# Optimization experiments

Hardware: AMD Instinct MI355X
Metric: run time of the kernel (lower is better)

## Reference

```python
import jax, jax.numpy as jnp
import numpy as np
from jax import lax

# Fixed image shape (H, W) for all images, standard detection resize
H_IMG, W_IMG = 800.0, 1333.0
SCORE_THRESH = 0.05
NMS_THRESH = 0.5
DET_PER_IMG = 100
K_PRE = 2048  # NMS candidate budget per image (after score threshold)
BBOX_XFORM_CLIP = float(np.log(1000.0 / 16.0))
WX, WY, WW, WH = 10.0, 10.0, 5.0, 5.0  # bbox_reg_weights


def setup_inputs() -> dict:
    B, P, C = 8, 2000, 81
    key = jax.random.key(0)
    k1, k2, k3, k4 = jax.random.split(key, 4)
    class_logits = 2.0 * jax.random.normal(k1, (B * P, C), jnp.float32)
    box_regression = 0.5 * jax.random.normal(k2, (B * P, C * 4), jnp.float32)
    # valid proposal boxes inside the image: (x1,y1) + (w,h)
    xy = jax.random.uniform(k3, (B, P, 2), jnp.float32) * jnp.array([W_IMG - 128.0, H_IMG - 128.0], jnp.float32)
    wh = 1.0 + 127.0 * jax.random.uniform(k4, (B, P, 2), jnp.float32)
    proposals = jnp.concatenate([xy, xy + wh], axis=-1)
    return {"class_logits": class_logits, "box_regression": box_regression, "proposals": proposals}


def _decode(rel, boxes):
    # BoxCoder.decode: rel [N, C, 4], boxes [N, 4] -> [N, C, 4]
    w = boxes[:, 2] - boxes[:, 0]
    h = boxes[:, 3] - boxes[:, 1]
    cx = boxes[:, 0] + 0.5 * w
    cy = boxes[:, 1] + 0.5 * h
    dx = rel[..., 0] / WX
    dy = rel[..., 1] / WY
    dw = jnp.minimum(rel[..., 2] / WW, BBOX_XFORM_CLIP)
    dh = jnp.minimum(rel[..., 3] / WH, BBOX_XFORM_CLIP)
    pcx = dx * w[:, None] + cx[:, None]
    pcy = dy * h[:, None] + cy[:, None]
    pw = jnp.exp(dw) * w[:, None]
    ph = jnp.exp(dh) * h[:, None]
    return jnp.stack([pcx - 0.5 * pw, pcy - 0.5 * ph, pcx + 0.5 * pw, pcy + 0.5 * ph], axis=-1)


def _pairwise_iou(b):
    # b: [K, 4] -> [K, K]
    area = jnp.maximum(b[:, 2] - b[:, 0], 0.0) * jnp.maximum(b[:, 3] - b[:, 1], 0.0)
    lt = jnp.maximum(b[:, None, :2], b[None, :, :2])
    rb = jnp.minimum(b[:, None, 2:], b[None, :, 2:])
    wh = jnp.maximum(rb - lt, 0.0)
    inter = wh[..., 0] * wh[..., 1]
    union = area[:, None] + area[None, :] - inter
    return inter / jnp.maximum(union, 1e-9)


def _greedy_nms(boxes, valid):
    # boxes: [K, 4] sorted by score desc; valid: [K] bool. Exact greedy NMS.
    K = boxes.shape[0]
    iou = _pairwise_iou(boxes)
    idx = jnp.arange(K)

    def body(i, keep):
        sup = keep[i] & (iou[i] > NMS_THRESH) & (idx > i)
        return keep & ~sup

    return lax.fori_loop(0, K, body, valid)


def reference(class_logits, box_regression, proposals):
    B, P, _ = proposals.shape
    C = class_logits.shape[-1]
    # decode all class-specific boxes, softmax scores
    rel = box_regression.reshape(-1, C, 4)
    pred = _decode(rel, proposals.reshape(-1, 4)).reshape(B, P, C, 4)
    scores = jax.nn.softmax(class_logits, axis=-1).reshape(B, P, C)
    # drop background class 0
    M = P * (C - 1)
    boxes = pred[:, :, 1:, :].reshape(B, M, 4)
    scores = scores[:, :, 1:].reshape(B, M)
    labels = jnp.broadcast_to(jnp.arange(1, C)[None, None, :], (B, P, C - 1)).reshape(B, M)
    # clip to image
    x1 = jnp.clip(boxes[..., 0], 0.0, W_IMG)
    y1 = jnp.clip(boxes[..., 1], 0.0, H_IMG)
    x2 = jnp.clip(boxes[..., 2], 0.0, W_IMG)
    y2 = jnp.clip(boxes[..., 3], 0.0, H_IMG)
    boxes = jnp.stack([x1, y1, x2, y2], axis=-1)
    # score threshold + remove_small_boxes(min_size=0.01), as a validity mask
    valid = (scores > SCORE_THRESH) & ((x2 - x1) >= 0.01) & ((y2 - y1) >= 0.01)
    masked = jnp.where(valid, scores, -1.0)
    # top-K candidates per image (sorted desc -> NMS visiting order)
    top_s, top_i = lax.top_k(masked, K_PRE)
    top_b = jnp.take_along_axis(boxes, top_i[..., None], axis=1)
    top_l = jnp.take_along_axis(labels, top_i, axis=1)
    top_v = top_s > 0.0
    # batched_nms: per-class coordinate offsets so classes never overlap
    off = top_l.astype(jnp.float32) * (jnp.maximum(W_IMG, H_IMG) + 1.0)
    keep = jax.vmap(_greedy_nms)(top_b + off[..., None], top_v)
    final = jnp.where(keep, top_s, -1.0)
    det_s, det_i = lax.top_k(final, DET_PER_IMG)
    det_b = jnp.take_along_axis(top_b, det_i[..., None], axis=1)
    det_l = jnp.take_along_axis(top_l, det_i, axis=1)
    det_valid = det_s > 0.0  # padding slots have score -1
    return det_b, det_s, det_l, det_valid
```

## Files before the change

### kernel.cpp

```cpp
#include <hip/hip_runtime.h>
#include <cstdint>
#include <cstddef>

typedef unsigned long long u64;

constexpr int Bn   = 8;
constexpr int Pn   = 2000;
constexpr int Cn   = 81;
constexpr int CM1  = 80;
constexpr int KPRE = 2048;
constexpr int NDET = 100;
constexpr int SECP = 8;
constexpr int NSEC2 = Pn / SECP;
constexpr int SSLOT = 160;
constexpr int CAP  = 4096;
constexpr int NBINS = 5632;
constexpr int BINOFF = (122 << 10);
constexpr float W_IMG = 1333.0f;
constexpr float H_IMG = 800.0f;
constexpr float XFORM_CLIP = 4.135166556742356f;
constexpr float NMS_OFF = 1334.0f;

constexpr size_t OFF_HIST = 0;
constexpr size_t ZERO_BYTES = (size_t)Bn * NBINS * 4;
constexpr size_t OFF_SL   = ZERO_BYTES;
constexpr size_t OFF_SC   = OFF_SL + (size_t)Bn * NSEC2 * SSLOT * 8;
constexpr size_t OFF_CANDA = OFF_SC + (size_t)Bn * NSEC2 * 4;

__device__ __forceinline__ void decode_clip(const float4 rv, float w, float h,
                                            float cx, float cy, float out[4]) {
  float dx = rv.x / 10.0f;
  float dy = rv.y / 10.0f;
  float dw = fminf(rv.z / 5.0f, XFORM_CLIP);
  float dh = fminf(rv.w / 5.0f, XFORM_CLIP);
  float pcx = dx * w + cx;
  float pcy = dy * h + cy;
  float pw = expf(dw) * w;
  float ph = expf(dh) * h;
  out[0] = fminf(fmaxf(pcx - 0.5f * pw, 0.0f), W_IMG);
  out[1] = fminf(fmaxf(pcy - 0.5f * ph, 0.0f), H_IMG);
  out[2] = fminf(fmaxf(pcx + 0.5f * pw, 0.0f), W_IMG);
  out[3] = fminf(fmaxf(pcy + 0.5f * ph, 0.0f), H_IMG);
}

__device__ __forceinline__ int score_bin(unsigned bits) {
  int bin = (int)(bits >> 13) - BINOFF;
  return min(max(bin, 0), NBINS - 1);
}

__device__ __forceinline__ void key_decode(u64 key, int b,
                                           const float* __restrict__ reg,
                                           const float* __restrict__ props,
                                           float bx[4], int& label, float& sc) {
  sc = __uint_as_float((unsigned)(key >> 32));
  bx[0] = bx[1] = bx[2] = bx[3] = 0.0f;
  label = 0;
  if (key != 0ull) {
    int m = (int)(0xFFFFFFFFu - (unsigned)key);
    int p = m / CM1;
    int c = m - p * CM1 + 1;
    int nidx = b * Pn + p;
    const float4 pb = *reinterpret_cast<const float4*>(props + (size_t)nidx * 4);
    float w = pb.z - pb.x, h = pb.w - pb.y;
    float cx = pb.x + 0.5f * w, cy = pb.y + 0.5f * h;
    float4 rv = *reinterpret_cast<const float4*>(reg + (size_t)nidx * (Cn * 4) + c * 4);
    decode_clip(rv, w, h, cx, cy, bx);
    label = c;
  }
}

__global__ __launch_bounds__(256) void
k1_score(const float* __restrict__ logits, const float* __restrict__ reg,
         const float* __restrict__ props, u64* __restrict__ slices,
         int* __restrict__ scnt, int* __restrict__ hist) {
  int blk = blockIdx.x, t = threadIdx.x, lane = t & 63, wv = t >> 6;
  int b = blk / NSEC2, sec = blk % NSEC2;
  __shared__ u64 cbuf[SSLOT];
  __shared__ int cnt_sh;
  if (t == 0) cnt_sh = 0;
  __syncthreads();
  int* hrow = hist + (size_t)b * NBINS;

  #pragma unroll
  for (int pp = wv; pp < SECP; pp += 4) {
    int p = sec * SECP + pp;
    int wid = b * Pn + p;
    const float* lg = logits + (size_t)wid * Cn;
    float x0 = lg[lane];
    float x1 = (lane < Cn - 64) ? lg[64 + lane] : -3.4e38f;
    float mx = fmaxf(x0, x1);
    for (int m = 32; m; m >>= 1) mx = fmaxf(mx, __shfl_xor(mx, m, 64));
    float e0 = expf(x0 - mx);
    float e1 = (lane < Cn - 64) ? expf(x1 - mx) : 0.0f;
    float ssum = e0 + e1;
    for (int m = 32; m; m >>= 1) ssum += __shfl_xor(ssum, m, 64);

    const float4 pb = *reinterpret_cast<const float4*>(props + (size_t)wid * 4);
    float w = pb.z - pb.x, h = pb.w - pb.y;
    float cx = pb.x + 0.5f * w, cy = pb.y + 0.5f * h;
    const float* rrow = reg + (size_t)wid * (Cn * 4);

    u64 key0 = 0ull, key1 = 0ull;
    if (lane >= 1) {
      float sc = e0 / ssum;
      if (sc > 0.05f) {
        float4 rv = *reinterpret_cast<const float4*>(rrow + lane * 4);
        float bx[4];
        decode_clip(rv, w, h, cx, cy, bx);
        if ((bx[2] - bx[0] >= 0.01f) && (bx[3] - bx[1] >= 0.01f)) {
          unsigned m = (unsigned)(p * CM1 + (lane - 1));
          key0 = ((u64)__float_as_uint(sc) << 32) | (0xFFFFFFFFu - m);
        }
      }
    }
    if (lane < Cn - 64) {
      int c = 64 + lane;
      float sc = e1 / ssum;
      if (sc > 0.05f) {
        float4 rv = *reinterpret_cast<const float4*>(rrow + c * 4);
        float bx[4];
        decode_clip(rv, w, h, cx, cy, bx);
        if ((bx[2] - bx[0] >= 0.01f) && (bx[3] - bx[1] >= 0.01f)) {
          unsigned m = (unsigned)(p * CM1 + (c - 1));
          key1 = ((u64)__float_as_uint(sc) << 32) | (0xFFFFFFFFu - m);
        }
      }
    }
    u64 bal0 = __ballot(key0 != 0ull);
    u64 bal1 = __ballot(key1 != 0ull);
    int tot = __popcll(bal0) + __popcll(bal1);
    if (tot) {
      int base = 0;
      if (lane == 0) base = atomicAdd(&cnt_sh, tot);
      base = __shfl(base, 0, 64);
      int r0 = __popcll(bal0 & ((1ull << lane) - 1ull));
      int r1 = __popcll(bal0) + __popcll(bal1 & ((1ull << lane) - 1ull));
      if (key0) {
        cbuf[base + r0] = key0;
        atomicAdd(&hrow[score_bin((unsigned)(key0 >> 32))], 1);
      }
      if (key1) {
        cbuf[base + r1] = key1;
        atomicAdd(&hrow[score_bin((unsigned)(key1 >> 32))], 1);
      }
    }
  }
  __syncthreads();
  int n = cnt_sh;
  for (int i = t; i < n; i += 256) slices[(size_t)blk * SSLOT + i] = cbuf[i];
  if (t == 0) scnt[blk] = n;
}

template <int CHV>
__device__ __forceinline__ void mp_round(u64* buf, int base, int nA, int nB,
                                         int outLen, int tid) {
  const u64* A = buf + base;
  const u64* B = buf + base + nA;
  int d = tid * CHV;
  u64 rg[CHV];
  int cnt = 0;
  if (d < outLen) {
    int lo = max(0, d - nB), hi = min(d, nA);
    while (lo < hi) {
      int mid = (lo + hi) >> 1;
      if (A[mid] >= B[d - 1 - mid]) lo = mid + 1; else hi = mid;
    }
    int i = lo, j = d - lo;
    for (int e = 0; e < CHV && d + e < outLen; e++) {
      u64 v;
      if (j >= nB || (i < nA && A[i] >= B[j])) v = A[i++];
      else v = B[j++];
      rg[cnt++] = v;
    }
  }
  __syncthreads();
  for (int e = 0; e < cnt; e++) buf[base + d + e] = rg[e];
  __syncthreads();
}

__global__ __launch_bounds__(1024) void
k2_fused(const int* __restrict__ hist, const u64* __restrict__ slices,
         const int* __restrict__ scnt, u64* __restrict__ candA,
         const float* __restrict__ reg, const float* __restrict__ props,
         float* __restrict__ out) {
  int b = blockIdx.x, t = threadIdx.x, lane = t & 63, w = t >> 6;
  __shared__ u64 bufA[CAP];
  __shared__ u64 maskb[256][4];
  __shared__ u64 keepw[KPRE / 64];
  __shared__ int accI[NDET];
  __shared__ int kcnt_sh;
  __shared__ int partial[256];
  __shared__ int sufAfter[256];
  __shared__ int lcnt[NSEC2];
  __shared__ int tmax_sh, cnt_sh;
  float4* obox = (float4*)bufA;

  for (int i = t; i < CAP; i += 1024) bufA[i] = 0ull;

  const int CH = NBINS / 256;
  const int* hrow = hist + (size_t)b * NBINS;
  if (t == 0) { tmax_sh = 0; cnt_sh = 0; }
  if (t < 256) {
    int lo = t * CH, hi = lo + CH;
    int s = 0;
    for (int i = lo; i < hi; i++) s += hrow[i];
    partial[t] = s;
  }
  if (t < NSEC2) lcnt[t] = scnt[b * NSEC2 + t];
  __syncthreads();
  if (t < 256) sufAfter[t] = partial[t];
  __syncthreads();
  for (int s = 1; s < 256; s <<= 1) {
    int y = 0;
    if (t < 256 && t + s < 256) y = sufAfter[t + s];
    __syncthreads();
    if (t < 256) sufAfter[t] += y;
    __syncthreads();
  }
  if (t < 256) {
    int lo = t * CH, hi = lo + CH;
    int cum = (t + 1 < 256) ? sufAfter[t + 1] : 0;
    int cand = -1;
    for (int i = hi - 1; i >= lo; i--) {
      cum += hrow[i];
      if (cum >= KPRE) { cand = i; break; }
    }
    if (cand >= 0) atomicMax(&tmax_sh, cand);
  }
  __syncthreads();
  int T = tmax_sh;

  for (int sec = w; sec < NSEC2; sec += 16) {
    int n = lcnt[sec];
    const u64* sl = slices + (size_t)(b * NSEC2 + sec) * SSLOT;
    for (int i0 = 0; i0 < n; i0 += 64) {
      int i = i0 + lane;
      u64 key = (i < n) ? sl[i] : 0ull;
      bool pass = key && (score_bin((unsigned)(key >> 32)) >= T);
      u64 bal = __ballot(pass);
      int tot = __popcll(bal);
      if (tot) {
        int base = 0;
        if (lane == 0) base = atomicAdd(&cnt_sh, tot);
        base = __shfl(base, 0, 64);
        int rank = __popcll(bal & ((1ull << lane) - 1ull));
        int pos = base + rank;
        if (pass && pos < CAP) bufA[pos] = key;
      }
    }
  }
  __syncthreads();
  int cnt = min(cnt_sh, CAP);
  int nch = (cnt + 511) >> 9;
  int lim = nch << 9;

  for (int k = 2; k <= 512; k <<= 1) {
    for (int j = k >> 1; j > 0; j >>= 1) {
      for (int i = t; i < lim; i += 1024) {
        int l = i & 511, cb = i & ~511;
        int lx = l ^ j;
        if (lx > l) {
          u64 a = bufA[cb | l], c2 = bufA[cb | lx];
          bool dir = ((l & k) == 0);
          if ((a < c2) == dir) { bufA[cb | l] = c2; bufA[cb | lx] = a; }
        }
      }
      __syncthreads();
    }
  }

  mp_round<4>(bufA, (t >> 8) * 1024, 512, 512, 1024, t & 255);
  mp_round<4>(bufA, (t >> 9) * 2048, 1024, 1024, 2048, t & 511);
  mp_round<2>(bufA, 0, 2048, 2048, 2048, t);

  u64 k0 = bufA[t], k1 = bufA[t + 1024];
  candA[(size_t)b * CAP + t] = k0;
  candA[(size_t)b * CAP + t + 1024] = k1;
  {
    u64 bal = __ballot(k0 != 0ull);
    if (lane == 0) keepw[w] = bal;
    bal = __ballot(k1 != 0ull);
    if (lane == 0) keepw[16 + w] = bal;
  }
  __syncthreads();
  #pragma unroll
  for (int s = 0; s < 2; s++) {
    int j = t + s * 1024;
    u64 key = s ? k1 : k0;
    float bx[4]; int label; float sc;
    key_decode(key, b, reg, props, bx, label, sc);
    float off = (float)label * NMS_OFF;
    obox[j] = make_float4(bx[0] + off, bx[1] + off, bx[2] + off, bx[3] + off);
  }
  __syncthreads();

  int kcount = 0;
  for (int w0 = 0; w0 < KPRE && kcount < NDET; w0 += 256) {
    if (w0 > 0 && kcount > 0) {
      if (t < 256) {
        int j = w0 + t;
        u64 kwv = keepw[j >> 6];
        bool alive = (kwv >> (j & 63)) & 1ull;
        if (alive) {
          float4 jb = obox[j];
          float jar = fmaxf(jb.z - jb.x, 0.0f) * fmaxf(jb.w - jb.y, 0.0f);
          for (int a = 0; a < kcount; a++) {
            float4 ab = obox[accI[a]];
            float ix1 = fmaxf(ab.x, jb.x), iy1 = fmaxf(ab.y, jb.y);
            float ix2 = fminf(ab.z, jb.z), iy2 = fminf(ab.w, jb.w);
            float iw = fmaxf(ix2 - ix1, 0.0f), ih = fmaxf(iy2 - iy1, 0.0f);
            float inter = iw * ih;
            if (inter > 0.0f) {
              float aar = fmaxf(ab.z - ab.x, 0.0f) * fmaxf(ab.w - ab.y, 0.0f);
              float iou = inter / fmaxf(aar + jar - inter, 1e-9f);
              if (iou > 0.5f) { alive = false; break; }
            }
          }
        }
        u64 bal = __ballot(alive);
        if (lane == 0) keepw[(w0 >> 6) + (t >> 6)] = bal;
      }
      __syncthreads();
    }
    {
      int r = t >> 2, wd = t & 3;
      int rgp = w0 + r;
      bool ralive = (keepw[rgp >> 6] >> (rgp & 63)) & 1ull;
      float4 rb = obox[rgp];
      float rar = fmaxf(rb.z - rb.x, 0.0f) * fmaxf(rb.w - rb.y, 0.0f);
      u64 m = 0;
      if (ralive) {
        int cb0 = w0 + wd * 64;
        for (int jj = 0; jj < 64; jj++) {
          int cg = cb0 + jj;
          float4 cb = obox[cg];
          float ix1 = fmaxf(rb.x, cb.x), iy1 = fmaxf(rb.y, cb.y);
          float ix2 = fminf(rb.z, cb.z), iy2 = fminf(rb.w, cb.w);
          float iw = fmaxf(ix2 - ix1, 0.0f), ih = fmaxf(iy2 - iy1, 0.0f);
          float inter = iw * ih;
          if (inter > 0.0f && cg > rgp) {
            float car = fmaxf(cb.z - cb.x, 0.0f) * fmaxf(cb.w - cb.y, 0.0f);
            float iou = inter / fmaxf(rar + car - inter, 1e-9f);
            if (iou > 0.5f) m |= (1ull << jj);
          }
        }
      }
      maskb[r][wd] = m;
    }
    __syncthreads();
    if (w == 0) {
      u64 kw0 = keepw[(w0 >> 6) + 0];
      u64 kw1 = keepw[(w0 >> 6) + 1];
      u64 kw2 = keepw[(w0 >> 6) + 2];
      u64 kw3 = keepw[(w0 >> 6) + 3];
      int kc = kcount;
      #pragma unroll
      for (int wq = 0; wq < 4; wq++) {
        u64 cw = (wq == 0) ? kw0 : (wq == 1) ? kw1 : (wq == 2) ? kw2 : kw3;
        if (cw == 0ull) continue;
        for (int rb0 = 0; rb0 < 64 && kc < NDET; rb0 += 4) {
          u64 gbits = (cw >> rb0) & 0xFull;
          int r = wq * 64 + rb0;
          u64 rm0a = maskb[r][0],   rm0b = maskb[r][1],   rm0c = maskb[r][2],   rm0d = maskb[r][3];
          u64 rm1a = maskb[r+1][0], rm1b = maskb[r+1][1], rm1c = maskb[r+1][2], rm1d = maskb[r+1][3];
          u64 rm2a = maskb[r+2][0], rm2b = maskb[r+2][1], rm2c = maskb[r+2][2], rm2d = maskb[r+2][3];
          u64 rm3a = maskb[r+3][0], rm3b = maskb[r+3][1], rm3c = maskb[r+3][2], rm3d = maskb[r+3][3];
          if (gbits == 0ull) continue;
          #pragma unroll
          for (int d = 0; d < 4; d++) {
            u64 cwq = (wq == 0) ? kw0 : (wq == 1) ? kw1 : (wq == 2) ? kw2 : kw3;
            if ((cwq >> (rb0 + d)) & 1ull) {
              if (lane == 0) accI[kc] = w0 + r + d;
              kc++;
              if (kc >= NDET) break;
              u64 ma = (d == 0) ? rm0a : (d == 1) ? rm1a : (d == 2) ? rm2a : rm3a;
              u64 mb = (d == 0) ? rm0b : (d == 1) ? rm1b : (d == 2) ? rm2b : rm3b;
              u64 mc = (d == 0) ? rm0c : (d == 1) ? rm1c : (d == 2) ? rm2c : rm3c;
              u64 md = (d == 0) ? rm0d : (d == 1) ? rm1d : (d == 2) ? rm2d : rm3d;
              kw0 &= ~ma; kw1 &= ~mb; kw2 &= ~mc; kw3 &= ~md;
            }
          }
          cw = (wq == 0) ? kw0 : (wq == 1) ? kw1 : (wq == 2) ? kw2 : kw3;
        }
      }
      if (lane == 0) {
        keepw[(w0 >> 6) + 0] = kw0;
        keepw[(w0 >> 6) + 1] = kw1;
        keepw[(w0 >> 6) + 2] = kw2;
        keepw[(w0 >> 6) + 3] = kw3;
        kcnt_sh = kc;
      }
    }
    __syncthreads();
    kcount = kcnt_sh;
  }

  if (t == 0 && kcount < NDET) {
    int run = kcount;
    for (int wq = 0; wq < KPRE / 64 && run < NDET; wq++) {
      u64 nk = ~keepw[wq];
      while (nk && run < NDET) {
        int bit2 = __ffsll((long long)nk) - 1;
        nk &= nk - 1;
        accI[run++] = wq * 64 + bit2;
      }
    }
  }
  __syncthreads();

  if (t < NDET) {
    int k = accI[t];
    bool kept = t < kcount;
    u64 key = candA[(size_t)b * CAP + k];
    float bx[4]; int label; float sc;
    key_decode(key, b, reg, props, bx, label, sc);
    int oi = b * NDET + t;
    out[(size_t)oi * 4 + 0] = bx[0];
    out[(size_t)oi * 4 + 1] = bx[1];
    out[(size_t)oi * 4 + 2] = bx[2];
    out[(size_t)oi * 4 + 3] = bx[3];
    out[Bn * NDET * 4 + oi] = kept ? sc : -1.0f;
    out[Bn * NDET * 5 + oi] = (float)label;
    out[Bn * NDET * 6 + oi] = kept ? 1.0f : 0.0f;
  }
}

extern "C" void kernel_launch(void* const* d_in, const int* in_sizes, int n_in,
                              void* d_out, int out_size, void* d_ws, size_t ws_size,
                              hipStream_t stream) {
  const float* logits = (const float*)d_in[0];
  const float* reg    = (const float*)d_in[1];
  const float* props  = (const float*)d_in[2];
  float* out = (float*)d_out;
  char* ws = (char*)d_ws;

  int* hist   = (int*)(ws + OFF_HIST);
  u64* slices = (u64*)(ws + OFF_SL);
  int* scnt   = (int*)(ws + OFF_SC);
  u64* candA  = (u64*)(ws + OFF_CANDA);

  hipMemsetAsync(ws + OFF_HIST, 0, ZERO_BYTES, stream);
  k1_score<<<Bn * NSEC2, 256, 0, stream>>>(logits, reg, props, slices, scnt, hist);
  k2_fused<<<Bn, 1024, 0, stream>>>(hist, slices, scnt, candA, reg, props, out);
}
```

Before: 144.4 us.

## Compact candidates globally per image and sort with wave shuffles plus segmented merges

The score kernel now appends candidate keys straight to a per-image global array through a global atomic counter. This replaces the per-block shared-memory slices and counts, and removes one block barrier and the copy-out. The select kernel caches the histogram in LDS and does the suffix scan with wave shuffles instead of a barrier-heavy loop. It gathers candidates with a prefetched strided loop, sorts 64-key runs in registers with shuffle bitonic networks, then merges them with segmented merge-path rounds that skip empty segments. Kept keys stay in LDS instead of going through global candA, at the cost of global atomic contention in the score kernel and more LDS use.

```diff
diff --git a/kernel.cpp b/kernel.cpp
--- a/kernel.cpp
+++ b/kernel.cpp
@@ -12,8 +12,8 @@
 constexpr int NDET = 100;
 constexpr int SECP = 8;
 constexpr int NSEC2 = Pn / SECP;
-constexpr int SSLOT = 160;
 constexpr int CAP  = 4096;
+constexpr int ACAP = 38400;
 constexpr int NBINS = 5632;
 constexpr int BINOFF = (122 << 10);
 constexpr float W_IMG = 1333.0f;
@@ -22,10 +22,9 @@
 constexpr float NMS_OFF = 1334.0f;
 
 constexpr size_t OFF_HIST = 0;
-constexpr size_t ZERO_BYTES = (size_t)Bn * NBINS * 4;
-constexpr size_t OFF_SL   = ZERO_BYTES;
-constexpr size_t OFF_SC   = OFF_SL + (size_t)Bn * NSEC2 * SSLOT * 8;
-constexpr size_t OFF_CANDA = OFF_SC + (size_t)Bn * NSEC2 * 4;
+constexpr size_t OFF_GCNT = (size_t)Bn * NBINS * 4;
+constexpr size_t ZERO_BYTES = OFF_GCNT + (size_t)Bn * 4;
+constexpr size_t OFF_CALL = ZERO_BYTES;
 
 __device__ __forceinline__ void decode_clip(const float4 rv, float w, float h,
                                             float cx, float cy, float out[4]) {
@@ -71,15 +70,12 @@
 
 __global__ __launch_bounds__(256) void
 k1_score(const float* __restrict__ logits, const float* __restrict__ reg,
-         const float* __restrict__ props, u64* __restrict__ slices,
-         int* __restrict__ scnt, int* __restrict__ hist) {
+         const float* __restrict__ props, u64* __restrict__ candAll,
+         int* __restrict__ gcnt, int* __restrict__ hist) {
   int blk = blockIdx.x, t = threadIdx.x, lane = t & 63, wv = t >> 6;
   int b = blk / NSEC2, sec = blk % NSEC2;
-  __shared__ u64 cbuf[SSLOT];
-  __shared__ int cnt_sh;
-  if (t == 0) cnt_sh = 0;
-  __syncthreads();
   int* hrow = hist + (size_t)b * NBINS;
+  u64* crow = candAll + (size_t)b * ACAP;
 
   #pragma unroll
   for (int pp = wv; pp < SECP; pp += 4) {
@@ -131,24 +127,20 @@
     int tot = __popcll(bal0) + __popcll(bal1);
     if (tot) {
       int base = 0;
-      if (lane == 0) base = atomicAdd(&cnt_sh, tot);
+      if (lane == 0) base = atomicAdd(&gcnt[b], tot);
       base = __shfl(base, 0, 64);
       int r0 = __popcll(bal0 & ((1ull << lane) - 1ull));
       int r1 = __popcll(bal0) + __popcll(bal1 & ((1ull << lane) - 1ull));
       if (key0) {
-        cbuf[base + r0] = key0;
+        crow[base + r0] = key0;
         atomicAdd(&hrow[score_bin((unsigned)(key0 >> 32))], 1);
       }
       if (key1) {
-        cbuf[base + r1] = key1;
+        crow[base + r1] = key1;
         atomicAdd(&hrow[score_bin((unsigned)(key1 >> 32))], 1);
       }
     }
   }
-  __syncthreads();
-  int n = cnt_sh;
-  for (int i = t; i < n; i += 256) slices[(size_t)blk * SSLOT + i] = cbuf[i];
-  if (t == 0) scnt[blk] = n;
 }
 
 template <int CHV>
@@ -178,51 +170,90 @@
   __syncthreads();
 }
 
+template <int CHV>
+__device__ __forceinline__ void mp_seg_round(u64* buf, int len, int cnt, int t) {
+  int tps = len / CHV;
+  int seg = t / tps;
+  int tid = t - seg * tps;
+  int base = seg * len;
+  bool act = (base < cnt);
+  int nA = len >> 1;
+  int d = tid * CHV;
+  u64 rg[CHV];
+  if (act) {
+    const u64* A = buf + base;
+    const u64* B = buf + base + nA;
+    int lo = max(0, d - nA), hi = min(d, nA);
+    while (lo < hi) {
+      int mid = (lo + hi) >> 1;
+      if (A[mid] >= B[d - 1 - mid]) lo = mid + 1; else hi = mid;
+    }
+    int i = lo, j = d - lo;
+    #pragma unroll
+    for (int e = 0; e < CHV; e++) {
+      u64 v;
+      if (j >= nA || (i < nA && A[i] >= B[j])) v = A[i++];
+      else v = B[j++];
+      rg[e] = v;
+    }
+  }
+  __syncthreads();
+  if (act) {
+    #pragma unroll
+    for (int e = 0; e < CHV; e++) buf[base + d + e] = rg[e];
+  }
+  __syncthreads();
+}
+
 __global__ __launch_bounds__(1024) void
-k2_fused(const int* __restrict__ hist, const u64* __restrict__ slices,
-         const int* __restrict__ scnt, u64* __restrict__ candA,
-         const float* __restrict__ reg, const float* __restrict__ props,
-         float* __restrict__ out) {
+k2_fused(const int* __restrict__ hist, const u64* __restrict__ candAll,
+         const int* __restrict__ gcnt, const float* __restrict__ reg,
+         const float* __restrict__ props, float* __restrict__ out) {
   int b = blockIdx.x, t = threadIdx.x, lane = t & 63, w = t >> 6;
   __shared__ u64 bufA[CAP];
+  __shared__ u64 keys2[KPRE];
   __shared__ u64 maskb[256][4];
   __shared__ u64 keepw[KPRE / 64];
   __shared__ int accI[NDET];
-  __shared__ int kcnt_sh;
-  __shared__ int partial[256];
+  __shared__ int hlds[NBINS];
   __shared__ int sufAfter[256];
-  __shared__ int lcnt[NSEC2];
-  __shared__ int tmax_sh, cnt_sh;
+  __shared__ int chunkTot[4];
+  __shared__ int tmax_sh, cnt_sh, kcnt_sh;
   float4* obox = (float4*)bufA;
 
-  for (int i = t; i < CAP; i += 1024) bufA[i] = 0ull;
-
-  const int CH = NBINS / 256;
   const int* hrow = hist + (size_t)b * NBINS;
   if (t == 0) { tmax_sh = 0; cnt_sh = 0; }
+  for (int i = t; i < NBINS; i += 1024) hlds[i] = hrow[i];
+  for (int i = t; i < CAP; i += 1024) bufA[i] = 0ull;
+  __syncthreads();
+
+  const int CH = NBINS / 256;
+  int suf = 0;
   if (t < 256) {
-    int lo = t * CH, hi = lo + CH;
+    int lo = t * CH;
     int s = 0;
-    for (int i = lo; i < hi; i++) s += hrow[i];
-    partial[t] = s;
-  }
-  if (t < NSEC2) lcnt[t] = scnt[b * NSEC2 + t];
-  __syncthreads();
-  if (t < 256) sufAfter[t] = partial[t];
-  __syncthreads();
-  for (int s = 1; s < 256; s <<= 1) {
-    int y = 0;
-    if (t < 256 && t + s < 256) y = sufAfter[t + s];
-    __syncthreads();
-    if (t < 256) sufAfter[t] += y;
-    __syncthreads();
-  }
+    #pragma unroll
+    for (int i = 0; i < CH; i++) s += hlds[lo + i];
+    for (int d2 = 1; d2 < 64; d2 <<= 1) {
+      int v = __shfl_down(s, d2, 64);
+      if (lane + d2 < 64) s += v;
+    }
+    if (lane == 0) chunkTot[t >> 6] = s;
+    suf = s;
+  }
+  __syncthreads();
+  if (t < 256) {
+    int w4 = t >> 6;
+    for (int q = w4 + 1; q < 4; q++) suf += chunkTot[q];
+    sufAfter[t] = suf;
+  }
+  __syncthreads();
   if (t < 256) {
     int lo = t * CH, hi = lo + CH;
     int cum = (t + 1 < 256) ? sufAfter[t + 1] : 0;
     int cand = -1;
     for (int i = hi - 1; i >= lo; i--) {
-      cum += hrow[i];
+      cum += hlds[i];
       if (cum >= KPRE) { cand = i; break; }
     }
     if (cand >= 0) atomicMax(&tmax_sh, cand);
@@ -230,12 +261,15 @@
   __syncthreads();
   int T = tmax_sh;
 
-  for (int sec = w; sec < NSEC2; sec += 16) {
-    int n = lcnt[sec];
-    const u64* sl = slices + (size_t)(b * NSEC2 + sec) * SSLOT;
-    for (int i0 = 0; i0 < n; i0 += 64) {
-      int i = i0 + lane;
-      u64 key = (i < n) ? sl[i] : 0ull;
+  int n = min(gcnt[b], ACAP);
+  const u64* crow = candAll + (size_t)b * ACAP;
+  {
+    int i0 = t & ~63;
+    u64 nxt = (i0 + lane < n) ? crow[i0 + lane] : 0ull;
+    for (; i0 < n; i0 += 1024) {
+      u64 key = nxt;
+      int j0 = i0 + 1024;
+      nxt = (j0 + lane < n) ? crow[j0 + lane] : 0ull;
       bool pass = key && (score_bin((unsigned)(key >> 32)) >= T);
       u64 bal = __ballot(pass);
       int tot = __popcll(bal);
@@ -251,42 +285,47 @@
   }
   __syncthreads();
   int cnt = min(cnt_sh, CAP);
-  int nch = (cnt + 511) >> 9;
-  int lim = nch << 9;
-
-  for (int k = 2; k <= 512; k <<= 1) {
-    for (int j = k >> 1; j > 0; j >>= 1) {
-      for (int i = t; i < lim; i += 1024) {
-        int l = i & 511, cb = i & ~511;
-        int lx = l ^ j;
-        if (lx > l) {
-          u64 a = bufA[cb | l], c2 = bufA[cb | lx];
-          bool dir = ((l & k) == 0);
-          if ((a < c2) == dir) { bufA[cb | l] = c2; bufA[cb | lx] = a; }
-        }
-      }
-      __syncthreads();
-    }
-  }
-
-  mp_round<4>(bufA, (t >> 8) * 1024, 512, 512, 1024, t & 255);
-  mp_round<4>(bufA, (t >> 9) * 2048, 1024, 1024, 2048, t & 511);
-  mp_round<2>(bufA, 0, 2048, 2048, 2048, t);
-
-  u64 k0 = bufA[t], k1 = bufA[t + 1024];
-  candA[(size_t)b * CAP + t] = k0;
-  candA[(size_t)b * CAP + t + 1024] = k1;
+
+  for (int r = w; (r << 6) < cnt; r += 16) {
+    u64 v = bufA[(r << 6) | lane];
+    #pragma unroll
+    for (int k = 2; k <= 64; k <<= 1) {
+      #pragma unroll
+      for (int j = k >> 1; j > 0; j >>= 1) {
+        u64 o = __shfl_xor(v, j, 64);
+        bool dir = ((lane & k) == 0);
+        bool lower = ((lane & j) == 0);
+        u64 mn = (v < o) ? v : o;
+        u64 mx = (v < o) ? o : v;
+        v = (dir == lower) ? mx : mn;
+      }
+    }
+    bufA[(r << 6) | lane] = v;
+  }
+  __syncthreads();
+
+  mp_seg_round<4>(bufA, 128, cnt, t);
+  mp_seg_round<4>(bufA, 256, cnt, t);
+  mp_seg_round<4>(bufA, 512, cnt, t);
+  mp_seg_round<4>(bufA, 1024, cnt, t);
+  mp_seg_round<4>(bufA, 2048, cnt, t);
+  if (cnt > 2048)
+    mp_round<2>(bufA, 0, 2048, 2048, 2048, t);
+
+  u64 k0 = bufA[t], k1v = bufA[t + 1024];
+  keys2[t] = k0;
+  keys2[t + 1024] = k1v;
   {
     u64 bal = __ballot(k0 != 0ull);
     if (lane == 0) keepw[w] = bal;
-    bal = __ballot(k1 != 0ull);
+    bal = __ballot(k1v != 0ull);
     if (lane == 0) keepw[16 + w] = bal;
   }
   __syncthreads();
   #pragma unroll
   for (int s = 0; s < 2; s++) {
     int j = t + s * 1024;
-    u64 key = s ? k1 : k0;
+    u64 key = s ? k1v : k0;
     float bx[4]; int label; float sc;
     key_decode(key, b, reg, props, bx, label, sc);
     float off = (float)label * NMS_OFF;
@@ -411,7 +450,7 @@
   if (t < NDET) {
     int k = accI[t];
     bool kept = t < kcount;
-    u64 key = candA[(size_t)b * CAP + k];
+    u64 key = keys2[k];
     float bx[4]; int label; float sc;
     key_decode(key, b, reg, props, bx, label, sc);
     int oi = b * NDET + t;
@@ -434,12 +473,11 @@
   float* out = (float*)d_out;
   char* ws = (char*)d_ws;
 
-  int* hist   = (int*)(ws + OFF_HIST);
-  u64* slices = (u64*)(ws + OFF_SL);
-  int* scnt   = (int*)(ws + OFF_SC);
-  u64* candA  = (u64*)(ws + OFF_CANDA);
+  int* hist    = (int*)(ws + OFF_HIST);
+  int* gcnt    = (int*)(ws + OFF_GCNT);
+  u64* candAll = (u64*)(ws + OFF_CALL);
 
   hipMemsetAsync(ws + OFF_HIST, 0, ZERO_BYTES, stream);
-  k1_score<<<Bn * NSEC2, 256, 0, stream>>>(logits, reg, props, slices, scnt, hist);
-  k2_fused<<<Bn, 1024, 0, stream>>>(hist, slices, scnt, candA, reg, props, out);
-}
+  k1_score<<<Bn * NSEC2, 256, 0, stream>>>(logits, reg, props, candAll, gcnt, hist);
+  k2_fused<<<Bn, 1024, 0, stream>>>(hist, candAll, gcnt, reg, props, out);
+}
```

New measurement: 302.4 us. +109.4%, slower.
